# Optimization experiments

Hardware: AMD Instinct MI355X
Metric: run time of the kernel (lower is better)

The kernel has to match this reference:

```python
import jax, jax.numpy as jnp
import numpy as np
from jax import lax

IMG = 512            # image H = W
FH = FW = 32         # feature map spatial size
A = 9                # anchors per location (3 sizes x 3 ratios)
N = FH * FW * A      # total anchors = 9216
IOU_THR = 0.7
MIN_SCORE = 0.5
MIN_SIZE = 1e-3


def make_anchors():
    """Anchors in centroid format (cx, cy, w, h), ordered (H, W, A)."""
    stride = IMG / FH
    sizes = np.array([32.0, 64.0, 128.0])
    ratios = np.array([0.5, 1.0, 2.0])
    ws = (sizes[:, None] / np.sqrt(ratios)[None, :]).reshape(-1)  # (A,)
    hs = (sizes[:, None] * np.sqrt(ratios)[None, :]).reshape(-1)  # (A,)
    cx = (np.arange(FW) + 0.5) * stride
    cy = (np.arange(FH) + 0.5) * stride
    CX = np.broadcast_to(cx[None, :, None], (FH, FW, A))
    CY = np.broadcast_to(cy[:, None, None], (FH, FW, A))
    Wg = np.broadcast_to(ws[None, None, :], (FH, FW, A))
    Hg = np.broadcast_to(hs[None, None, :], (FH, FW, A))
    anc = np.stack([CX, CY, Wg, Hg], axis=-1).reshape(-1, 4)
    return jnp.asarray(anc, dtype=jnp.float32)


def pairwise_iou(b):
    # b: (N,4) corners x1,y1,x2,y2
    x1, y1, x2, y2 = b[:, 0], b[:, 1], b[:, 2], b[:, 3]
    area = (x2 - x1) * (y2 - y1)
    ix1 = jnp.maximum(x1[:, None], x1[None, :])
    iy1 = jnp.maximum(y1[:, None], y1[None, :])
    ix2 = jnp.minimum(x2[:, None], x2[None, :])
    iy2 = jnp.minimum(y2[:, None], y2[None, :])
    inter = jnp.maximum(ix2 - ix1, 0.0) * jnp.maximum(iy2 - iy1, 0.0)
    union = area[:, None] + area[None, :] - inter
    return inter / jnp.maximum(union, 1e-9)


def nms_keep(boxes, scores, valid):
    """Greedy NMS. Returns bool keep mask of shape (N,). Index decisions only."""
    s = jnp.where(valid, scores, -jnp.inf)
    order = jnp.argsort(-s)
    b = boxes[order]
    v = valid[order]
    ious = pairwise_iou(b)  # (N, N)
    idx = jnp.arange(N)

    def body(i, supp):
        keep_i = (~supp[i]) & v[i]
        return supp | (keep_i & (ious[i] > IOU_THR) & (idx > i))

    supp = lax.fori_loop(0, N, body, jnp.zeros(N, dtype=bool))
    keep_sorted = (~supp) & v
    return jnp.zeros(N, dtype=bool).at[order].set(keep_sorted)


def setup_inputs() -> dict:
    key = jax.random.key(0)
    ks = jax.random.split(key, 4)
    return {
        "feature_map": jax.random.normal(ks[0], (1, 256, FH, FW), jnp.float32),
        "conv1_w": jax.random.normal(ks[1], (512, 256, 3, 3), jnp.float32) * 0.02,
        "conv1_b": jnp.zeros((512,), jnp.float32),
        "conv2_w": jax.random.normal(ks[2], (A, 512), jnp.float32) * 0.01,
        "conv2_b": jnp.zeros((A,), jnp.float32),
        "conv3_w": jax.random.normal(ks[3], (4 * A, 512), jnp.float32) * 0.01,
        "conv3_b": jnp.zeros((4 * A,), jnp.float32),
    }


def reference(feature_map, conv1_w, conv1_b, conv2_w, conv2_b, conv3_w, conv3_b):
    anchors = make_anchors()  # (N,4) cx,cy,w,h

    # --- conv backbone head ---
    h = lax.conv_general_dilated(
        feature_map, conv1_w, (1, 1), "SAME",
        dimension_numbers=("NCHW", "OIHW", "NCHW"))
    h = jax.nn.relu(h + conv1_b[None, :, None, None])  # (1,512,H,W)

    scores = jax.nn.sigmoid(
        jnp.einsum("bchw,ac->bahw", h, conv2_w) + conv2_b[None, :, None, None])
    scores = scores.transpose(0, 2, 3, 1).reshape(-1)  # (N,) ordered (H,W,A)

    off = jnp.einsum("bchw,oc->bohw", h, conv3_w) + conv3_b[None, :, None, None]
    off = off.reshape(1, A, 4, FH, FW).transpose(0, 3, 4, 1, 2).reshape(-1, 4)

    acx, acy, aw, ah = anchors[:, 0], anchors[:, 1], anchors[:, 2], anchors[:, 3]
    cx = acx + off[:, 0] * aw
    cy = acy + off[:, 1] * ah
    bw = aw * jnp.exp(off[:, 2])
    bh = ah * jnp.exp(off[:, 3])
    boxes = jnp.stack([cx - bw / 2, cy - bh / 2, cx + bw / 2, cy + bh / 2], axis=1)

    # --- clip to image ---
    lo = jnp.array([0.0, 0.0, 0.0, 0.0], jnp.float32)
    hi = jnp.array([IMG, IMG, IMG, IMG], jnp.float32)
    boxes = jnp.clip(boxes, lo, hi)

    # --- remove small boxes + score threshold (as a mask, jit-safe) ---
    valid = ((boxes[:, 2] - boxes[:, 0]) >= MIN_SIZE) \
          & ((boxes[:, 3] - boxes[:, 1]) >= MIN_SIZE) \
          & (scores >= MIN_SCORE)

    # --- NMS (selection is index-based; no gradient through the decision) ---
    keep = nms_keep(lax.stop_gradient(boxes), lax.stop_gradient(scores), valid)

    out = jnp.concatenate(
        [boxes * keep[:, None].astype(boxes.dtype),
         (scores * keep.astype(scores.dtype))[:, None]], axis=1)  # (N,5)
    return out
```

## Files before the change

### kernel.cpp

```cpp
#include <hip/hip_runtime.h>
#include <math.h>

#define FHW   32
#define NA    9
#define NBOX  9216
#define C1    256
#define C2    512
#define KTOT  2304
#define KS    8
#define KCH   (KTOT / KS)
#define CAP   64
#define ECAP  16384
#define ROUNDS 96

struct AnchorWH { float w[NA]; float h[NA]; };

#define FP_OFF    0u
#define WT_OFF    1183744u
#define HP_OFF    5902336u
#define BOX_OFF   22679552u
#define SC_OFF    22827008u
#define VL_OFF    22863872u
#define DEG_OFF   22900736u
#define ADJ_OFF   22937600u
#define KEEP_OFF  24117248u
#define NV_OFF    24154112u

__global__ __launch_bounds__(256) void k_prep(const float* __restrict__ fin,
                                              float* __restrict__ Fp,
                                              unsigned int* __restrict__ deg,
                                              unsigned int* __restrict__ keepG,
                                              unsigned int* __restrict__ nv,
                                              const float* __restrict__ w1,
                                              float* __restrict__ Wt) {
    if (blockIdx.x < 1156) {
        int idx = blockIdx.x * 256 + threadIdx.x;
        if (idx < 256 * 34 * 34) {
            int c   = idx / 1156;
            int rem = idx - c * 1156;
            int yy  = rem / 34;
            int xx  = rem - yy * 34;
            float v = 0.f;
            if (yy >= 1 && yy <= 32 && xx >= 1 && xx <= 32)
                v = fin[c * 1024 + (yy - 1) * 32 + (xx - 1)];
            Fp[idx] = v;
        }
        if (idx < NBOX) { deg[idx] = 0u; keepG[idx] = 0u; }
        if (idx == 0)   *nv = 0u;
    } else {
        __shared__ float tile[32][33];
        int tb  = blockIdx.x - 1156;
        int k0  = (tb % 72) * 32;
        int oc0 = (tb / 72) * 32;
        int t   = threadIdx.x;
        int r0 = t >> 5, c = t & 31;
        #pragma unroll
        for (int i = 0; i < 4; ++i) {
            int r = r0 + 8 * i;
            tile[r][c] = w1[(oc0 + r) * KTOT + k0 + c];
        }
        __syncthreads();
        #pragma unroll
        for (int i = 0; i < 4; ++i) {
            int kk = r0 + 8 * i;
            Wt[(k0 + kk) * C2 + oc0 + c] = tile[c][kk];
        }
    }
}

__global__ __launch_bounds__(256, 2) void k_gemm(const float* __restrict__ Fp,
                                                 const float* __restrict__ Wt,
                                                 float* __restrict__ hp) {
    const int id = blockIdx.x;
    const int bx = id >> 5, g = id & 31;
    const int by = g >> 3, kz = g & 7;
    const int p0  = bx * 64;
    const int oc0 = by * 128;
    const int k0b = kz * KCH;
    const int t  = threadIdx.x;
    const int ty = t >> 4, tx = t & 15;

    __shared__ float As[16][64];
    __shared__ float Bs[16][128];

    float acc[4][8];
    #pragma unroll
    for (int r = 0; r < 4; ++r)
        #pragma unroll
        for (int c = 0; c < 8; ++c) acc[r][c] = 0.f;

    for (int kt = 0; kt < KCH; kt += 16) {
        #pragma unroll
        for (int i = 0; i < 4; ++i) {
            int e  = t + 256 * i;
            int kk = e >> 6, pp = e & 63;
            int k   = k0b + kt + kk;
            int c   = k / 9;
            int kap = k - c * 9;
            int dy  = kap / 3;
            int dx  = kap - dy * 3;
            int p  = p0 + pp;
            int y  = p >> 5, x = p & 31;
            As[kk][pp] = Fp[(c * 34 + y + dy) * 34 + x + dx];
        }
        #pragma unroll
        for (int i = 0; i < 2; ++i) {
            int e4 = t + 256 * i;
            int kk = e4 >> 5, c4 = e4 & 31;
            *(float4*)&Bs[kk][c4 * 4] =
                *(const float4*)&Wt[(k0b + kt + kk) * C2 + oc0 + c4 * 4];
        }
        __syncthreads();
        #pragma unroll
        for (int kk = 0; kk < 16; ++kk) {
            float a[4], b[8];
            *(float4*)&a[0] = *(const float4*)&As[kk][ty * 4];
            *(float4*)&b[0] = *(const float4*)&Bs[kk][tx * 4];
            *(float4*)&b[4] = *(const float4*)&Bs[kk][tx * 4 + 64];
            #pragma unroll
            for (int r = 0; r < 4; ++r)
                #pragma unroll
                for (int c = 0; c < 8; ++c) acc[r][c] += a[r] * b[c];
        }
        __syncthreads();
    }
    #pragma unroll
    for (int r = 0; r < 4; ++r) {
        int p = p0 + ty * 4 + r;
        float* dst = hp + ((kz * 1024 + p) * C2 + oc0 + tx * 4);
        *(float4*)dst        = *(float4*)&acc[r][0];
        *(float4*)(dst + 64) = *(float4*)&acc[r][4];
    }
}

__global__ __launch_bounds__(256) void k_heads(const float* __restrict__ hp,
                                               const float* __restrict__ b1,
                                               const float* __restrict__ w2,
                                               const float* __restrict__ b2,
                                               const float* __restrict__ w3,
                                               const float* __restrict__ b3,
                                               float* __restrict__ boxes,
                                               float* __restrict__ scoresG,
                                               unsigned int* __restrict__ nv,
                                               unsigned int* __restrict__ vlist,
                                               AnchorWH awh) {
    const int p0 = blockIdx.x * 4;
    const int t  = threadIdx.x;
    __shared__ float hrow[4][C2];
    __shared__ float arr[4][45];

    #pragma unroll
    for (int px = 0; px < 4; ++px) {
        int p = p0 + px;
        #pragma unroll
        for (int i = 0; i < 2; ++i) {
            int c = t + 256 * i;
            float s = b1[c];
            #pragma unroll
            for (int ks = 0; ks < KS; ++ks) s += hp[(ks * 1024 + p) * C2 + c];
            hrow[px][c] = fmaxf(s, 0.f);
        }
    }
    __syncthreads();

    const int w = t >> 6, lane = t & 63;
    for (int job = w; job < 180; job += 4) {
        int px = job / 45, j = job - px * 45;
        const float* wp = (j < 9) ? (w2 + j * C2) : (w3 + (j - 9) * C2);
        float s = 0.f;
        #pragma unroll
        for (int i = 0; i < 8; ++i) s += hrow[px][lane + 64 * i] * wp[lane + 64 * i];
        #pragma unroll
        for (int d = 1; d < 64; d <<= 1) s += __shfl_xor(s, d, 64);
        if (lane == 0) arr[px][j] = s;
    }
    __syncthreads();

    if (t < 36) {
        int px = t / 9, a = t - px * 9;
        int p = p0 + px;
        float logit = arr[px][a] + b2[a];
        float score = 1.f / (1.f + expf(-logit));
        float o0 = arr[px][9 + a * 4 + 0] + b3[a * 4 + 0];
        float o1 = arr[px][9 + a * 4 + 1] + b3[a * 4 + 1];
        float o2 = arr[px][9 + a * 4 + 2] + b3[a * 4 + 2];
        float o3 = arr[px][9 + a * 4 + 3] + b3[a * 4 + 3];
        int y = p >> 5, x = p & 31;
        float ax = (x + 0.5f) * 16.f, ay = (y + 0.5f) * 16.f;
        float aw = awh.w[a], ah = awh.h[a];
        float cx = ax + o0 * aw;
        float cy = ay + o1 * ah;
        float bw = aw * expf(o2);
        float bh = ah * expf(o3);
        float x1 = fminf(fmaxf(cx - bw * 0.5f, 0.f), 512.f);
        float y1 = fminf(fmaxf(cy - bh * 0.5f, 0.f), 512.f);
        float x2 = fminf(fmaxf(cx + bw * 0.5f, 0.f), 512.f);
        float y2 = fminf(fmaxf(cy + bh * 0.5f, 0.f), 512.f);
        int n = p * 9 + a;
        float4 bx4; bx4.x = x1; bx4.y = y1; bx4.z = x2; bx4.w = y2;
        ((float4*)boxes)[n] = bx4;
        scoresG[n] = score;
        bool valid = (x2 - x1 >= 0.001f) && (y2 - y1 >= 0.001f) && (score >= 0.5f);
        if (valid) {
            unsigned int ci = atomicAdd(nv, 1u);
            vlist[ci] = (unsigned int)n;
        }
    }
}

__global__ __launch_bounds__(256) void k_adj(const unsigned int* __restrict__ nvp,
                                             const unsigned int* __restrict__ vlist,
                                             const float* __restrict__ boxes,
                                             const float* __restrict__ scoresG,
                                             unsigned int* __restrict__ deg,
                                             unsigned short* __restrict__ adj) {
    const int Nv = (int)*nvp;
    int b = blockIdx.x;
    int tv = (int)(sqrtf(2.f * b + 0.25f) - 0.5f);
    while ((tv + 1) * (tv + 2) / 2 <= b) tv++;
    while (tv * (tv + 1) / 2 > b) tv--;
    int tu = b - tv * (tv + 1) / 2;
    if (tv * 128 >= Nv) return;

    __shared__ float4 ub[128], vb[128];
    __shared__ float  us[128], vs[128];
    __shared__ int    uo[128], vo[128];
    int t = threadIdx.x;
    if (t < 128) {
        int gi = tu * 128 + t;
        if (gi < Nv) { int n = (int)vlist[gi]; ub[t] = ((const float4*)boxes)[n]; us[t] = scoresG[n]; uo[t] = n; }
        else us[t] = -1.f;
    } else {
        int tt = t - 128;
        int gj = tv * 128 + tt;
        if (gj < Nv) { int n = (int)vlist[gj]; vb[tt] = ((const float4*)boxes)[n]; vs[tt] = scoresG[n]; vo[tt] = n; }
        else vs[tt] = -1.f;
    }
    __syncthreads();

    for (int s = 0; s < 64; ++s) {
        int q  = t + 256 * s;
        int i  = q >> 7, jj = q & 127;
        if (tu == tv && i >= jj) continue;
        float su = us[i], sv = vs[jj];
        if (su < 0.f || sv < 0.f) continue;
        float4 bu = ub[i], bv = vb[jj];
        float au = (bu.z - bu.x) * (bu.w - bu.y);
        float av = (bv.z - bv.x) * (bv.w - bv.y);
        float ix1 = fmaxf(bu.x, bv.x), iy1 = fmaxf(bu.y, bv.y);
        float ix2 = fminf(bu.z, bv.z), iy2 = fminf(bu.w, bv.w);
        float inter = fmaxf(ix2 - ix1, 0.f) * fmaxf(iy2 - iy1, 0.f);
        float uni = au + av - inter;
        float iou = inter / fmaxf(uni, 1e-9f);
        if (iou > 0.7f) {
            int gi = tu * 128 + i, gj = tv * 128 + jj;
            bool uHigh = (su > sv) || (su == sv && uo[i] < vo[jj]);
            int lower = uHigh ? gj : gi;
            int upper = uHigh ? gi : gj;
            unsigned int slot = atomicAdd(&deg[lower], 1u);
            if (slot < CAP) adj[lower * CAP + slot] = (unsigned short)upper;
        }
    }
}

__global__ __launch_bounds__(512) void k_peel(const unsigned int* __restrict__ nvp,
                                              const unsigned int* __restrict__ vlist,
                                              const unsigned int* __restrict__ degG,
                                              const unsigned short* __restrict__ adjG,
                                              unsigned int* __restrict__ keepG) {
    __shared__ unsigned short offL[NBOX + 2];
    __shared__ unsigned char  st[NBOX];
    __shared__ unsigned short csr[ECAP];
    __shared__ unsigned int   scratch[512];
    __shared__ unsigned char  flags[ROUNDS];
    const int t  = threadIdx.x;
    const int Nv = (int)*nvp;
    const int chunk = (Nv + 511) / 512;
    const int i0 = t * chunk;
    const int i1 = (i0 + chunk < Nv) ? (i0 + chunk) : Nv;

    if (t < ROUNDS) flags[t] = 0;

    unsigned int lsum = 0;
    for (int i = i0; i < i1; ++i) {
        unsigned int d = degG[i];
        if (d > CAP) d = CAP;
        st[i] = (unsigned char)d;
        lsum += d;
    }
    scratch[t] = lsum;
    __syncthreads();
    for (int ofs = 1; ofs < 512; ofs <<= 1) {
        unsigned int v = (t >= ofs) ? scratch[t - ofs] : 0u;
        __syncthreads();
        scratch[t] += v;
        __syncthreads();
    }
    if (t == 511) {
        unsigned int tot = scratch[511];
        offL[Nv] = (unsigned short)(tot < ECAP ? tot : ECAP);
    }
    unsigned int amask = 0;
    {
        unsigned int off = scratch[t] - lsum;
        for (int i = i0; i < i1; ++i) {
            unsigned int o = (off < ECAP) ? off : ECAP;
            offL[i] = (unsigned short)o;
            int d = st[i];
            int ld = (int)ECAP - (int)o; if (ld > d) ld = d; if (ld < 0) ld = 0;
            for (int s = 0; s < ld; ++s)
                csr[o + s] = adjG[i * CAP + s];
            off += d;
            if (d == 0) st[i] = 1;
            else { st[i] = 0; amask |= 1u << (i - i0); }
        }
    }
    __syncthreads();

    for (int r = 0; r < ROUNDS; ++r) {
        bool any = false;
        unsigned int m = amask;
        while (m) {
            int b = __ffs(m) - 1; m &= m - 1;
            int i = i0 + b;
            int o = offL[i], on = offL[i + 1];
            int d, ld;
            if (on < ECAP) { d = on - o; ld = d; }
            else {
                unsigned int dg = degG[i]; d = (dg > CAP) ? CAP : (int)dg;
                ld = (int)ECAP - o; if (ld < 0) ld = 0; if (ld > d) ld = d;
            }
            bool kseen = false, useen = false;
            for (int s = 0; s < d; ++s) {
                int j = (s < ld) ? (int)csr[o + s] : (int)adjG[i * CAP + s];
                unsigned char v = st[j];
                kseen |= (v == 1);
                useen |= (v == 0);
            }
            if (kseen)       { st[i] = 2; any = true; amask &= ~(1u << b); }
            else if (!useen) { st[i] = 1; any = true; amask &= ~(1u << b); }
        }
        if (any) flags[r] = 1;
        __syncthreads();
        if (!flags[r]) break;
    }

    for (int i = i0; i < i1; ++i)
        if (st[i] == 1) keepG[vlist[i]] = 1u;
}

__global__ __launch_bounds__(256) void k_out(const float* __restrict__ boxes,
                                             const float* __restrict__ scoresG,
                                             const unsigned int* __restrict__ keepG,
                                             float* __restrict__ out) {
    int n = blockIdx.x * 256 + threadIdx.x;
    if (n >= NBOX) return;
    float k = keepG[n] ? 1.f : 0.f;
    float4 b = ((const float4*)boxes)[n];
    out[n * 5 + 0] = b.x * k;
    out[n * 5 + 1] = b.y * k;
    out[n * 5 + 2] = b.z * k;
    out[n * 5 + 3] = b.w * k;
    out[n * 5 + 4] = scoresG[n] * k;
}

extern "C" void kernel_launch(void* const* d_in, const int* in_sizes, int n_in,
                              void* d_out, int out_size, void* d_ws, size_t ws_size,
                              hipStream_t stream) {
    const float* fin = (const float*)d_in[0];
    const float* w1  = (const float*)d_in[1];
    const float* b1  = (const float*)d_in[2];
    const float* w2  = (const float*)d_in[3];
    const float* b2  = (const float*)d_in[4];
    const float* w3  = (const float*)d_in[5];
    const float* b3  = (const float*)d_in[6];
    float* out = (float*)d_out;

    char* ws = (char*)d_ws;
    float*          Fp    = (float*)(ws + FP_OFF);
    float*          Wt    = (float*)(ws + WT_OFF);
    float*          hp    = (float*)(ws + HP_OFF);
    float*          boxes = (float*)(ws + BOX_OFF);
    float*          sc    = (float*)(ws + SC_OFF);
    unsigned int*   vlist = (unsigned int*)(ws + VL_OFF);
    unsigned int*   deg   = (unsigned int*)(ws + DEG_OFF);
    unsigned short* adj   = (unsigned short*)(ws + ADJ_OFF);
    unsigned int*   keepG = (unsigned int*)(ws + KEEP_OFF);
    unsigned int*   nv    = (unsigned int*)(ws + NV_OFF);

    AnchorWH awh;
    {
        const double sizes[3]  = {32.0, 64.0, 128.0};
        const double ratios[3] = {0.5, 1.0, 2.0};
        for (int si = 0; si < 3; ++si)
            for (int ri = 0; ri < 3; ++ri) {
                awh.w[si * 3 + ri] = (float)(sizes[si] / sqrt(ratios[ri]));
                awh.h[si * 3 + ri] = (float)(sizes[si] * sqrt(ratios[ri]));
            }
    }

    k_prep<<<dim3(1156 + 72 * 16), 256, 0, stream>>>(fin, Fp, deg, keepG, nv, w1, Wt);
    k_gemm<<<dim3(512), 256, 0, stream>>>(Fp, Wt, hp);
    k_heads<<<dim3(256), 256, 0, stream>>>(hp, b1, w2, b2, w3, b3, boxes, sc, nv, vlist, awh);
    k_adj<<<dim3(72 * 73 / 2), 256, 0, stream>>>(nv, vlist, boxes, sc, deg, adj);
    k_peel<<<dim3(1), 512, 0, stream>>>(nv, vlist, deg, adj, keepG);
    k_out<<<dim3((NBOX + 255) / 256), 256, 0, stream>>>(boxes, sc, keepG, out);
}
```

Before: 204.7 us.

## Reorder weight K by tap-major and prefetch GEMM tiles through registers

The weight transpose now stores the reduction dimension as tap-major (tap*256+channel), so each K slice of the implicit-im2col GEMM has a fixed (dy,dx) shift. This removes the per-element div/mod index math from the A loads. The GEMM K tile grows from 16 to 32, and the next tile is loaded into registers while the current tile is computed. This is meant to hide global load latency and halve the number of barrier pairs. The cost is more shared memory and register pressure, which could reduce occupancy under launch_bounds(256,2).

```diff
diff --git a/kernel.cpp b/kernel.cpp
--- a/kernel.cpp
+++ b/kernel.cpp
@@ -62,8 +62,11 @@
         __syncthreads();
         #pragma unroll
         for (int i = 0; i < 4; ++i) {
-            int kk = r0 + 8 * i;
-            Wt[(k0 + kk) * C2 + oc0 + c] = tile[c][kk];
+            int kk  = r0 + 8 * i;
+            int k   = k0 + kk;
+            int ch  = k / 9;
+            int kap = k - ch * 9;
+            Wt[(kap * 256 + ch) * C2 + oc0 + c] = tile[c][kk];
         }
     }
 }
@@ -80,8 +83,14 @@
     const int t  = threadIdx.x;
     const int ty = t >> 4, tx = t & 15;
 
-    __shared__ float As[16][64];
-    __shared__ float Bs[16][128];
+    __shared__ float As[32][64];
+    __shared__ float Bs[32][128];
+
+    const int pp   = t & 63;
+    const int kkA0 = t >> 6;
+    const int kkB0 = t >> 5;
+    const int c4   = (t & 31) << 2;
+    const int yx   = ((p0 + pp) >> 5) * 34 + ((p0 + pp) & 31);
 
     float acc[4][8];
     #pragma unroll
@@ -89,30 +98,33 @@
         #pragma unroll
         for (int c = 0; c < 8; ++c) acc[r][c] = 0.f;
 
-    for (int kt = 0; kt < KCH; kt += 16) {
-        #pragma unroll
-        for (int i = 0; i < 4; ++i) {
-            int e  = t + 256 * i;
-            int kk = e >> 6, pp = e & 63;
-            int k   = k0b + kt + kk;
-            int c   = k / 9;
-            int kap = k - c * 9;
-            int dy  = kap / 3;
-            int dx  = kap - dy * 3;
-            int p  = p0 + pp;
-            int y  = p >> 5, x = p & 31;
-            As[kk][pp] = Fp[(c * 34 + y + dy) * 34 + x + dx];
-        }
-        #pragma unroll
-        for (int i = 0; i < 2; ++i) {
-            int e4 = t + 256 * i;
-            int kk = e4 >> 5, c4 = e4 & 31;
-            *(float4*)&Bs[kk][c4 * 4] =
-                *(const float4*)&Wt[(k0b + kt + kk) * C2 + oc0 + c4 * 4];
-        }
-        __syncthreads();
-        #pragma unroll
-        for (int kk = 0; kk < 16; ++kk) {
+    float  aS[8];
+    float4 bS[4];
+
+    auto LOAD = [&](int s) {
+        int tap = s >> 8, c0 = s & 255;
+        int dy  = (tap * 11) >> 5;
+        int dx  = tap - 3 * dy;
+        const float* ab = Fp + (c0 * 34 + dy) * 34 + dx + yx;
+        #pragma unroll
+        for (int i = 0; i < 8; ++i) aS[i] = ab[(kkA0 + 4 * i) * 1156];
+        const float* bb = Wt + (s + kkB0) * C2 + oc0 + c4;
+        #pragma unroll
+        for (int i = 0; i < 4; ++i) bS[i] = *(const float4*)(bb + (8 * i) * C2);
+    };
+
+    LOAD(k0b);
+    #pragma unroll 1
+    for (int kt = 0; kt < KCH; kt += 32) {
+        __syncthreads();
+        #pragma unroll
+        for (int i = 0; i < 8; ++i) As[kkA0 + 4 * i][pp] = aS[i];
+        #pragma unroll
+        for (int i = 0; i < 4; ++i) *(float4*)&Bs[kkB0 + 8 * i][c4] = bS[i];
+        __syncthreads();
+        if (kt + 32 < KCH) LOAD(k0b + kt + 32);
+        #pragma unroll
+        for (int kk = 0; kk < 32; ++kk) {
             float a[4], b[8];
             *(float4*)&a[0] = *(const float4*)&As[kk][ty * 4];
             *(float4*)&b[0] = *(const float4*)&Bs[kk][tx * 4];
@@ -122,7 +134,6 @@
                 #pragma unroll
                 for (int c = 0; c < 8; ++c) acc[r][c] += a[r] * b[c];
         }
-        __syncthreads();
     }
     #pragma unroll
     for (int r = 0; r < 4; ++r) {
@@ -327,7 +338,7 @@
             int d, ld;
             if (on < ECAP) { d = on - o; ld = d; }
             else {
-                unsigned int dg = degG[i]; d = (dg > CAP) ? CAP : (int)dg;
+            unsigned int dg = degG[i]; d = (dg > CAP) ? CAP : (int)dg;
                 ld = (int)ECAP - o; if (ld < 0) ld = 0; if (ld > d) ld = d;
             }
             bool kseen = false, useen = false;
```

After: 203.5 us. Within noise of the previous version (-0.6%).
